# Kernel tuning notes

Measured on AMD Instinct MI355X. Metric: run time of the kernel, lower is better.

The kernel has to match this reference:

```python
import jax, jax.numpy as jnp
import numpy as np
import math

D_MODEL = 1024
NUM_HEADS = 16
B, L = 2, 2048
# scale_level=0, patch_time_span=1 -> effective_stride=1
PERIODS = (1.0, 30.0)
WEIGHTS = (0.8, 0.4)
SIGMAS = (0.5, 2.0)


def setup_inputs() -> dict:
    key = jax.random.key(0)
    ks = jax.random.split(key, 10)
    s = 1.0 / math.sqrt(D_MODEL)
    inp = {
        "x": jax.random.normal(ks[0], (B, L, D_MODEL), dtype=jnp.float32),
        "Wq": jax.random.normal(ks[1], (D_MODEL, D_MODEL), dtype=jnp.float32) * s,
        "bq": jax.random.normal(ks[2], (D_MODEL,), dtype=jnp.float32) * 0.01,
        "Wk": jax.random.normal(ks[3], (D_MODEL, D_MODEL), dtype=jnp.float32) * s,
        "bk": jax.random.normal(ks[4], (D_MODEL,), dtype=jnp.float32) * 0.01,
        "Wv": jax.random.normal(ks[5], (D_MODEL, D_MODEL), dtype=jnp.float32) * s,
        "bv": jax.random.normal(ks[6], (D_MODEL,), dtype=jnp.float32) * 0.01,
        "Wo": jax.random.normal(ks[7], (D_MODEL, D_MODEL), dtype=jnp.float32) * s,
        "bo": jax.random.normal(ks[8], (D_MODEL,), dtype=jnp.float32) * 0.01,
        "prior_lambda": jnp.asarray(2.0, dtype=jnp.float32),
    }
    return inp


def _gaussian_mask(length):
    idx = jnp.arange(length, dtype=jnp.float32)
    delta = jnp.abs(idx[:, None] - idx[None, :])  # [L, L]
    mask = jnp.zeros_like(delta)
    for p, w, sigma in zip(PERIODS, WEIGHTS, SIGMAS):
        if p < 0.2:
            continue
        mask = mask + w * jnp.exp(-((delta - p) ** 2) / (2.0 * sigma ** 2))
    return mask


def reference(x, Wq, bq, Wk, bk, Wv, bv, Wo, bo, prior_lambda):
    Bx, Lx, D = x.shape
    H = NUM_HEADS
    hd = D // H

    def split_heads(t):  # [B, L, D] -> [B, H, L, hd]
        return t.reshape(Bx, Lx, H, hd).transpose(0, 2, 1, 3)

    Q = split_heads(x @ Wq.T + bq)
    K = split_heads(x @ Wk.T + bk)
    V = split_heads(x @ Wv.T + bv)

    scores = jnp.einsum("bhqd,bhkd->bhqk", Q, K) / math.sqrt(hd)
    scores = scores + prior_lambda * _gaussian_mask(Lx)[None, None, :, :]
    attn = jax.nn.softmax(scores, axis=-1)
    out = jnp.einsum("bhqk,bhkd->bhqd", attn, V)
    out = out.transpose(0, 2, 1, 3).reshape(Bx, Lx, D)
    return out @ Wo.T + bo
```

## Files before the change

kernel.cpp:

```cpp
#include <hip/hip_runtime.h>

#define D_MODEL 1024
#define SEQ_L   2048
#define NHEADS  16
#define HDIM    64
#define NROWS   4096

#define QSCALE 0.18033688011112042f
#define LOG2E  1.4426950408889634f

#if __has_builtin(__builtin_amdgcn_exp2f)
#define EXP2F(x) __builtin_amdgcn_exp2f(x)
#else
#define EXP2F(x) __expf((x) * 0.6931471805599453f)
#endif

typedef __attribute__((ext_vector_type(8))) short short8;
typedef __attribute__((ext_vector_type(4))) short short4v;
typedef __attribute__((ext_vector_type(4))) float floatx4;
typedef __attribute__((ext_vector_type(4))) unsigned short ushort4v;
typedef unsigned short ushort;

static __device__ __forceinline__ ushort f2bf(float f) {
    unsigned int u = __float_as_uint(f);
    u += 0x7FFFu + ((u >> 16) & 1u);
    return (ushort)(u >> 16);
}

static __device__ __forceinline__ floatx4 mfma16(short8 a, short8 b, floatx4 c) {
    return __builtin_amdgcn_mfma_f32_16x16x32_bf16(a, b, c, 0, 0, 0);
}

static __device__ __forceinline__ void store8bf(ushort* dst, float4 a, float4 b) {
    uint4 pk;
    pk.x = (unsigned)f2bf(a.x) | ((unsigned)f2bf(a.y) << 16);
    pk.y = (unsigned)f2bf(a.z) | ((unsigned)f2bf(a.w) << 16);
    pk.z = (unsigned)f2bf(b.x) | ((unsigned)f2bf(b.y) << 16);
    pk.w = (unsigned)f2bf(b.z) | ((unsigned)f2bf(b.w) << 16);
    *(uint4*)dst = pk;
}

static __device__ __forceinline__ void gll16(const ushort* g, ushort* l) {
    __builtin_amdgcn_global_load_lds(
        (const __attribute__((address_space(1))) unsigned int*)(const unsigned int*)g,
        (__attribute__((address_space(3))) unsigned int*)(unsigned int*)l,
        16, 0, 0);
}

__global__ __launch_bounds__(256) void convert_bf16(
    const float* __restrict__ x,
    const float* __restrict__ wq, const float* __restrict__ wk,
    const float* __restrict__ wv, const float* __restrict__ wo,
    ushort* __restrict__ xb, ushort* __restrict__ wb3, ushort* __restrict__ wob)
{
    const int seg = blockIdx.y;
    const float* src;
    ushort* dst;
    int n;
    if      (seg == 0) { src = x;  dst = xb;                n = 4194304; }
    else if (seg == 1) { src = wq; dst = wb3;               n = 1048576; }
    else if (seg == 2) { src = wk; dst = wb3 + 1048576;     n = 1048576; }
    else if (seg == 3) { src = wv; dst = wb3 + 2097152;     n = 1048576; }
    else               { src = wo; dst = wob;               n = 1048576; }
    const int i = (blockIdx.x * 256 + threadIdx.x) * 8;
    if (i >= n) return;
    float4 a = *(const float4*)(src + i);
    float4 b = *(const float4*)(src + i + 4);
    store8bf(dst + i, a, b);
}

__global__ __launch_bounds__(256, 4) void gemm_qkv(
    const ushort* __restrict__ A, const ushort* __restrict__ B,
    const float* __restrict__ bq, const float* __restrict__ bk,
    const float* __restrict__ bv,
    ushort* __restrict__ Qo, ushort* __restrict__ Ko, ushort* __restrict__ Vo)
{
    __shared__ ushort As[64 * 64];
    __shared__ ushort Bs[128 * 64];

    const int tid  = threadIdx.x;
    const int w    = tid >> 6;
    const int lane = tid & 63;
    const int l15  = lane & 15;
    const int quad = lane >> 4;

    const int bm = blockIdx.y * 64;
    const int bn = blockIdx.x * 128;
    const int z  = blockIdx.x >> 3;

    const int ciA0 = tid,        ciA1 = tid + 256;
    const int rA0 = ciA0 >> 3,   rA1 = ciA1 >> 3;
    const int sA0i = ciA0 & 7,   sA1i = ciA1 & 7;
    const ushort* aP0 = A + (size_t)(bm + rA0) * 1024 + (sA0i ^ (rA0 & 7)) * 8;
    const ushort* aP1 = A + (size_t)(bm + rA1) * 1024 + (sA1i ^ (rA1 & 7)) * 8;
    ushort* lA0 = &As[rA0 * 64 + sA0i * 8];
    ushort* lA1 = &As[rA1 * 64 + sA1i * 8];

    const ushort* bP[4];
    ushort* lB[4];
#pragma unroll
    for (int p = 0; p < 4; p++) {
        const int ci = tid + p * 256;
        const int r = ci >> 3, s = ci & 7;
        bP[p] = B + (size_t)(bn + r) * 1024 + (s ^ (r & 7)) * 8;
        lB[p] = &Bs[r * 64 + s * 8];
    }

    const int x7 = l15 & 7;

    floatx4 acc[4][2];
#pragma unroll
    for (int i = 0; i < 4; i++)
#pragma unroll
        for (int j = 0; j < 2; j++) acc[i][j] = (floatx4){0.f, 0.f, 0.f, 0.f};

    for (int k0 = 0; k0 < 1024; k0 += 64) {
        __syncthreads();
        gll16(aP0 + k0, lA0);
        gll16(aP1 + k0, lA1);
#pragma unroll
        for (int p = 0; p < 4; p++) gll16(bP[p] + k0, lB[p]);
        __syncthreads();

#pragma unroll
        for (int kk = 0; kk < 2; kk++) {
            const int slot = ((kk * 4 + quad) ^ x7) * 8;
            short8 af[4], bf[2];
#pragma unroll
            for (int mi = 0; mi < 4; mi++)
                af[mi] = *(const short8*)&As[(mi * 16 + l15) * 64 + slot];
#pragma unroll
            for (int ni = 0; ni < 2; ni++)
                bf[ni] = *(const short8*)&Bs[(w * 32 + ni * 16 + l15) * 64 + slot];
            if (z == 2) {
#pragma unroll
                for (int mi = 0; mi < 4; mi++)
#pragma unroll
                    for (int ni = 0; ni < 2; ni++)
                        acc[mi][ni] = mfma16(af[mi], bf[ni], acc[mi][ni]);
            } else {
#pragma unroll
                for (int mi = 0; mi < 4; mi++)
#pragma unroll
                    for (int ni = 0; ni < 2; ni++)
                        acc[mi][ni] = mfma16(bf[ni], af[mi], acc[mi][ni]);
            }
        }
    }

    __syncthreads();
    ushort* St = Bs;
    const int cwbase = bn & 1023;
    const int bb = bm >> 11;

    if (z == 2) {
#pragma unroll
        for (int ni = 0; ni < 2; ni++) {
            const int hdp = w * 32 + ni * 16 + l15;
            const float bvl = bv[cwbase + hdp];
            const int xr = (hdp & 7) << 1;
#pragma unroll
            for (int mi = 0; mi < 4; mi++) {
                ushort4v pk;
#pragma unroll
                for (int r = 0; r < 4; r++) pk[r] = f2bf(acc[mi][ni][r] + bvl);
                const int gs = (mi * 4 + quad) ^ xr;
                *(ushort4v*)&St[hdp * 64 + gs * 4] = pk;
            }
        }
        __syncthreads();
        const int li0 = bm & 2047;
        const int c = lane & 7;
#pragma unroll
        for (int t = 0; t < 4; t++) {
            const int hdp = w * 32 + t * 8 + (lane >> 3);
            const int h  = (cwbase >> 6) + (hdp >> 6);
            const int hd = hdp & 63;
            const int gs = (2 * c) ^ ((hdp & 7) << 1);
            uint4 vdat = *(const uint4*)&St[hdp * 64 + gs * 4];
            *(uint4*)(Vo + ((size_t)(bb * NHEADS + h) * HDIM + hd) * SEQ_L + li0 + c * 8) = vdat;
        }
    } else {
        const float* bias = z ? bk : bq;
        const float scale = z ? 1.0f : QSCALE;
        ushort* outp = z ? Ko : Qo;
#pragma unroll
        for (int ni = 0; ni < 2; ni++) {
            const int colw = cwbase + w * 32 + ni * 16 + quad * 4;
            const float4 bb4 = *(const float4*)&bias[colw];
#pragma unroll
            for (int mi = 0; mi < 4; mi++) {
                const int row = mi * 16 + l15;
                ushort4v pk;
                pk[0] = f2bf((acc[mi][ni][0] + bb4.x) * scale);
                pk[1] = f2bf((acc[mi][ni][1] + bb4.y) * scale);
                pk[2] = f2bf((acc[mi][ni][2] + bb4.z) * scale);
                pk[3] = f2bf((acc[mi][ni][3] + bb4.w) * scale);
                const int gs = (w * 8 + ni * 4 + quad) ^ ((row & 7) << 2);
                *(ushort4v*)&St[row * 128 + gs * 4] = pk;
            }
        }
        __syncthreads();
        const int c = l15;
        const int h0 = cwbase >> 6;
        const int h  = h0 + (c >> 3);
        const int hd0 = (c & 7) * 8;
#pragma unroll
        for (int t = 0; t < 4; t++) {
            const int row = w * 16 + t * 4 + quad;
            const int li = (bm + row) & 2047;
            const int gs = (2 * c) ^ ((row & 7) << 2);
            uint4 vdat = *(const uint4*)&St[row * 128 + gs * 4];
            *(uint4*)(outp + ((size_t)(bb * NHEADS + h) * SEQ_L + li) * HDIM + hd0) = vdat;
        }
    }
}

__global__ __launch_bounds__(256, 4) void attn(
    const ushort* __restrict__ Q,
    const ushort* __restrict__ K,
    const ushort* __restrict__ Vt,
    const float* __restrict__ lam,
    ushort* __restrict__ O0, ushort* __restrict__ O1,
    float* __restrict__ Lw)
{
    __shared__ float mtab[128];
    __shared__ ushort Ks[2][64 * 64];
    __shared__ ushort Vts[2][64 * 64];

    const int tid  = threadIdx.x;
    const int wave = tid >> 6;
    const int lane = tid & 63;
    const int l15  = lane & 15;
    const int quad = lane >> 4;

    const int qb = blockIdx.x;
    const int h  = blockIdx.y;
    const int zz = blockIdx.z;
    const int bz = zz >> 1;
    const int sp = zz & 1;
    const int bh = bz * NHEADS + h;
    const int q0 = qb * 128;
    const int kb = sp * 1024;

    const float lambda = *lam;
    if (tid < 128) {
        float d  = (float)tid;
        float e1 = (d - 1.f) * (d - 1.f);
        float e2 = (d - 30.f) * (d - 30.f);
        mtab[tid] = LOG2E * lambda *
                    (0.8f * __expf(-2.0f * e1) + 0.4f * __expf(-0.125f * e2));
    }

    const ushort* qp =
        Q + ((size_t)bh * SEQ_L + q0 + wave * 16 + l15) * HDIM + quad * 8;
    short8 qf[2][2];
    qf[0][0] = *(const short8*)qp;
    qf[0][1] = *(const short8*)(qp + 32);
    qf[1][0] = *(const short8*)(qp + 64 * HDIM);
    qf[1][1] = *(const short8*)(qp + 64 * HDIM + 32);

    const ushort* kbase = K  + ((size_t)bh * SEQ_L) * HDIM;
    const ushort* vbase = Vt + ((size_t)bh * HDIM) * SEQ_L;

    const int cid0 = tid, cid1 = 256 + tid;
    const int row0 = cid0 >> 3, row1 = cid1 >> 3;
    const int cl0  = (cid0 & 7) ^ (row0 & 7);
    const int cl1  = (cid1 & 7) ^ (row1 & 7);
    const ushort* kg0 = kbase + (size_t)(kb + row0) * HDIM + cl0 * 8;
    const ushort* kg1 = kbase + (size_t)(kb + row1) * HDIM + cl1 * 8;
    const ushort* vg0 = vbase + (size_t)row0 * SEQ_L + kb + cl0 * 8;
    const ushort* vg1 = vbase + (size_t)row1 * SEQ_L + kb + cl1 * 8;

    floatx4 o[2][4];
#pragma unroll
    for (int g = 0; g < 2; g++)
#pragma unroll
        for (int i = 0; i < 4; i++) o[g][i] = (floatx4){0.f, 0.f, 0.f, 0.f};
    floatx4 ol[2];
    ol[0] = (floatx4){0.f, 0.f, 0.f, 0.f};
    ol[1] = (floatx4){0.f, 0.f, 0.f, 0.f};

    uint4 onesw;
    onesw.x = 0x3F803F80u; onesw.y = 0x3F803F80u;
    onesw.z = 0x3F803F80u; onesw.w = 0x3F803F80u;
    const short8 ones8 = __builtin_bit_cast(short8, onesw);

    gll16(kg0, &Ks[0][cid0 * 8]);
    gll16(kg1, &Ks[0][cid1 * 8]);
    gll16(vg0, &Vts[0][cid0 * 8]);
    gll16(vg1, &Vts[0][cid1 * 8]);

    const int xo = l15 & 7;

    for (int t = 0; t < 16; t++) {
        const int cur = t & 1;
        __syncthreads();
        if (t + 1 < 16) {
            const int nxt = cur ^ 1;
            const int koff = (t + 1) * 64;
            gll16(kg0 + (size_t)koff * HDIM, &Ks[nxt][cid0 * 8]);
            gll16(kg1 + (size_t)koff * HDIM, &Ks[nxt][cid1 * 8]);
            gll16(vg0 + koff, &Vts[nxt][cid0 * 8]);
            gll16(vg1 + koff, &Vts[nxt][cid1 * 8]);
        }

        floatx4 s[2][4];
#pragma unroll
        for (int g = 0; g < 2; g++)
#pragma unroll
            for (int i = 0; i < 4; i++) s[g][i] = (floatx4){0.f, 0.f, 0.f, 0.f};
#pragma unroll
        for (int kk = 0; kk < 2; kk++) {
#pragma unroll
            for (int nt = 0; nt < 4; nt++) {
                const int slot = (kk * 4 + quad) ^ xo;
                short8 kf = *(const short8*)&Ks[cur][(nt * 16 + l15) * 64 + slot * 8];
                s[0][nt] = mfma16(kf, qf[0][kk], s[0][nt]);
                s[1][nt] = mfma16(kf, qf[1][kk], s[1][nt]);
            }
        }

        const int j = sp * 16 + t;
#pragma unroll
        for (int g = 0; g < 2; g++) {
            const int tg = j - (qb * 2 + g);
            if (tg >= -1 && tg <= 1) {
                const int qg = q0 + g * 64 + wave * 16 + l15;
#pragma unroll
                for (int nt = 0; nt < 4; nt++) {
                    const int kgi = j * 64 + nt * 16 + quad * 4;
#pragma unroll
                    for (int r = 0; r < 4; r++) {
                        int dq = qg - (kgi + r);
                        int ad = dq < 0 ? -dq : dq;
                        s[g][nt][r] += mtab[ad];
                    }
                }
            }
        }

        short8 pb8[2][2];
#pragma unroll
        for (int g = 0; g < 2; g++) {
#pragma unroll
            for (int c = 0; c < 2; c++) {
                unsigned ur[8];
#pragma unroll
                for (int r = 0; r < 4; r++)
                    ur[r] = __float_as_uint(EXP2F(s[g][2 * c][r])) + 0x8000u;
#pragma unroll
                for (int r = 0; r < 4; r++)
                    ur[4 + r] = __float_as_uint(EXP2F(s[g][2 * c + 1][r])) + 0x8000u;
                uint4 pk;
                pk.x = __builtin_amdgcn_perm(ur[1], ur[0], 0x07060302u);
                pk.y = __builtin_amdgcn_perm(ur[3], ur[2], 0x07060302u);
                pk.z = __builtin_amdgcn_perm(ur[5], ur[4], 0x07060302u);
                pk.w = __builtin_amdgcn_perm(ur[7], ur[6], 0x07060302u);
                pb8[g][c] = __builtin_bit_cast(short8, pk);
            }
        }

#pragma unroll
        for (int c = 0; c < 2; c++) {
#pragma unroll
            for (int nt = 0; nt < 4; nt++) {
                const int glo = ((c << 2) + (quad >> 1)) ^ xo;
                const int ghi = glo ^ 2;
                const int rb  = (nt * 16 + l15) * 64 + (quad & 1) * 4;
                short4v vlo = *(const short4v*)&Vts[cur][rb + glo * 8];
                short4v vhi = *(const short4v*)&Vts[cur][rb + ghi * 8];
                short8 vf8 = __builtin_shufflevector(vlo, vhi, 0, 1, 2, 3, 4, 5, 6, 7);
                o[0][nt] = mfma16(vf8, pb8[0][c], o[0][nt]);
                o[1][nt] = mfma16(vf8, pb8[1][c], o[1][nt]);
            }
            ol[0] = mfma16(ones8, pb8[0][c], ol[0]);
            ol[1] = mfma16(ones8, pb8[1][c], ol[1]);
        }
    }

    ushort* Osp = sp ? O1 : O0;
#pragma unroll
    for (int g = 0; g < 2; g++) {
        const int qg = q0 + g * 64 + wave * 16 + l15;
        if (quad == 0)
            Lw[((size_t)(sp * 2 + bz) * NHEADS + h) * SEQ_L + qg] = ol[g][0];
        ushort* obase = Osp + ((size_t)bz * SEQ_L + qg) * D_MODEL + h * HDIM;
#pragma unroll
        for (int nt = 0; nt < 4; nt++) {
            ushort4v pk;
#pragma unroll
            for (int r = 0; r < 4; r++) pk[r] = f2bf(o[g][nt][r]);
            *(ushort4v*)(obase + nt * 16 + quad * 4) = pk;
        }
    }
}

__global__ __launch_bounds__(256) void merge_attn(
    const ushort* __restrict__ O0, const ushort* __restrict__ O1,
    const float* __restrict__ Lw, ushort* __restrict__ Aout)
{
    const int gid = blockIdx.x * 256 + threadIdx.x;
    const int i = gid * 8;
    const int row = i >> 10;
    const int h   = (i >> 6) & 15;
    const int bz  = row >> 11, q = row & 2047;
    const int li  = (bz * NHEADS + h) * SEQ_L + q;
    const float linv = 1.f / (Lw[li] + Lw[2 * NHEADS * SEQ_L + li]);

    uint4 a = *(const uint4*)(O0 + i);
    uint4 b = *(const uint4*)(O1 + i);
    unsigned aw[4] = {a.x, a.y, a.z, a.w};
    unsigned bw[4] = {b.x, b.y, b.z, b.w};
    uint4 res;
    unsigned rw[4];
#pragma unroll
    for (int k = 0; k < 4; k++) {
        float alo = __uint_as_float(aw[k] << 16);
        float ahi = __uint_as_float(aw[k] & 0xFFFF0000u);
        float blo = __uint_as_float(bw[k] << 16);
        float bhi = __uint_as_float(bw[k] & 0xFFFF0000u);
        float lo = (alo + blo) * linv;
        float hi = (ahi + bhi) * linv;
        rw[k] = (unsigned)f2bf(lo) | ((unsigned)f2bf(hi) << 16);
    }
    res.x = rw[0]; res.y = rw[1]; res.z = rw[2]; res.w = rw[3];
    *(uint4*)(Aout + i) = res;
}

__global__ __launch_bounds__(256, 4) void gemm_out(
    const ushort* __restrict__ A, const ushort* __restrict__ B,
    const float* __restrict__ bo, float* __restrict__ out)
{
    __shared__ ushort As[64 * 64];
    __shared__ ushort Bs[64 * 64];

    const int tid  = threadIdx.x;
    const int w    = tid >> 6;
    const int lane = tid & 63;
    const int l15  = lane & 15;
    const int quad = lane >> 4;

    const int bm = blockIdx.y * 64;
    const int bn = blockIdx.x * 64;

    const int ci0 = tid, ci1 = tid + 256;
    const int r0 = ci0 >> 3, r1 = ci1 >> 3;
    const int s0 = ci0 & 7,  s1 = ci1 & 7;
    const ushort* aP0 = A + (size_t)(bm + r0) * 1024 + (s0 ^ (r0 & 7)) * 8;
    const ushort* aP1 = A + (size_t)(bm + r1) * 1024 + (s1 ^ (r1 & 7)) * 8;
    const ushort* bP0 = B + (size_t)(bn + r0) * 1024 + (s0 ^ (r0 & 7)) * 8;
    const ushort* bP1 = B + (size_t)(bn + r1) * 1024 + (s1 ^ (r1 & 7)) * 8;
    ushort* lA0 = &As[r0 * 64 + s0 * 8];
    ushort* lA1 = &As[r1 * 64 + s1 * 8];
    ushort* lB0 = &Bs[r0 * 64 + s0 * 8];
    ushort* lB1 = &Bs[r1 * 64 + s1 * 8];

    const int x7 = l15 & 7;

    floatx4 acc[4];
#pragma unroll
    for (int i = 0; i < 4; i++) acc[i] = (floatx4){0.f, 0.f, 0.f, 0.f};

    for (int k0 = 0; k0 < 1024; k0 += 64) {
        __syncthreads();
        gll16(aP0 + k0, lA0);
        gll16(aP1 + k0, lA1);
        gll16(bP0 + k0, lB0);
        gll16(bP1 + k0, lB1);
        __syncthreads();

#pragma unroll
        for (int kk = 0; kk < 2; kk++) {
            const int slot = ((kk * 4 + quad) ^ x7) * 8;
            short8 bf = *(const short8*)&Bs[(w * 16 + l15) * 64 + slot];
#pragma unroll
            for (int mi = 0; mi < 4; mi++) {
                short8 af = *(const short8*)&As[(mi * 16 + l15) * 64 + slot];
                acc[mi] = mfma16(bf, af, acc[mi]);
            }
        }
    }

    const int col0 = bn + w * 16 + quad * 4;
    const float4 bb4 = *(const float4*)&bo[col0];
#pragma unroll
    for (int mi = 0; mi < 4; mi++) {
        const int row = bm + mi * 16 + l15;
        float4 st;
        st.x = acc[mi][0] + bb4.x;
        st.y = acc[mi][1] + bb4.y;
        st.z = acc[mi][2] + bb4.z;
        st.w = acc[mi][3] + bb4.w;
        *(float4*)(out + (size_t)row * 1024 + col0) = st;
    }
}

extern "C" void kernel_launch(void* const* d_in, const int* in_sizes, int n_in,
                              void* d_out, int out_size, void* d_ws, size_t ws_size,
                              hipStream_t stream)
{
    const float* x   = (const float*)d_in[0];
    const float* Wq  = (const float*)d_in[1];
    const float* bq  = (const float*)d_in[2];
    const float* Wk  = (const float*)d_in[3];
    const float* bk  = (const float*)d_in[4];
    const float* Wv  = (const float*)d_in[5];
    const float* bv  = (const float*)d_in[6];
    const float* Wo  = (const float*)d_in[7];
    const float* bo  = (const float*)d_in[8];
    const float* lam = (const float*)d_in[9];
    float* out = (float*)d_out;

    const size_t NELEM = (size_t)NROWS * D_MODEL;
    ushort* Qw  = (ushort*)d_ws;
    ushort* Kw  = Qw + NELEM;
    ushort* Vw  = Kw + NELEM;
    ushort* O0  = Vw + NELEM;
    ushort* O1  = O0 + NELEM;
    ushort* XA  = O1 + NELEM;
    ushort* Wb3 = XA + NELEM;
    ushort* Wob = Wb3 + 3 * 1024 * 1024;
    float*  Lw  = (float*)(Wob + 1024 * 1024);

    dim3 gc(2048, 5);
    convert_bf16<<<gc, 256, 0, stream>>>(x, Wq, Wk, Wv, Wo, XA, Wb3, Wob);

    dim3 g1(3072 / 128, NROWS / 64);
    gemm_qkv<<<g1, 256, 0, stream>>>(XA, Wb3, bq, bk, bv, Qw, Kw, Vw);

    dim3 g2(SEQ_L / 128, NHEADS, 4);
    attn<<<g2, 256, 0, stream>>>(Qw, Kw, Vw, lam, O0, O1, Lw);

    merge_attn<<<NELEM / (256 * 8), 256, 0, stream>>>(O0, O1, Lw, XA);

    dim3 g3(1024 / 64, NROWS / 64);
    gemm_out<<<g3, 256, 0, stream>>>(XA, Wob, bo, out);
}
```

Before: 197.2 us.

## Drop split-K attention and merge kernel; use 64-row query tiles over full keys

The attention kernel stops splitting the key range into two halves that write partial outputs and row sums for a separate merge pass. Each block now handles 64 query rows over all 2048 keys and normalises in-register before writing bf16 output straight into the GEMM input buffer. This removes the merge kernel launch and the partial-output traffic. In exchange, K/V tiles loaded into shared memory are reused by half as many query rows, and the serial loop per block is twice as long, though the grid block count stays the same.

```diff
diff --git a/kernel.cpp b/kernel.cpp
--- a/kernel.cpp
+++ b/kernel.cpp
@@ -221,8 +221,7 @@
     const ushort* __restrict__ K,
     const ushort* __restrict__ Vt,
     const float* __restrict__ lam,
-    ushort* __restrict__ O0, ushort* __restrict__ O1,
-    float* __restrict__ Lw)
+    ushort* __restrict__ Aout)
 {
     __shared__ float mtab[128];
     __shared__ ushort Ks[2][64 * 64];
@@ -236,12 +235,9 @@
 
     const int qb = blockIdx.x;
     const int h  = blockIdx.y;
-    const int zz = blockIdx.z;
-    const int bz = zz >> 1;
-    const int sp = zz & 1;
+    const int bz = blockIdx.z;
     const int bh = bz * NHEADS + h;
-    const int q0 = qb * 128;
-    const int kb = sp * 1024;
+    const int q0 = qb * 64;
 
     const float lambda = *lam;
     if (tid < 128) {
@@ -254,11 +250,9 @@
 
     const ushort* qp =
         Q + ((size_t)bh * SEQ_L + q0 + wave * 16 + l15) * HDIM + quad * 8;
-    short8 qf[2][2];
-    qf[0][0] = *(const short8*)qp;
-    qf[0][1] = *(const short8*)(qp + 32);
-    qf[1][0] = *(const short8*)(qp + 64 * HDIM);
-    qf[1][1] = *(const short8*)(qp + 64 * HDIM + 32);
+    short8 qf[2];
+    qf[0] = *(const short8*)qp;
+    qf[1] = *(const short8*)(qp + 32);
 
     const ushort* kbase = K  + ((size_t)bh * SEQ_L) * HDIM;
     const ushort* vbase = Vt + ((size_t)bh * HDIM) * SEQ_L;
@@ -267,19 +261,15 @@
     const int row0 = cid0 >> 3, row1 = cid1 >> 3;
     const int cl0  = (cid0 & 7) ^ (row0 & 7);
     const int cl1  = (cid1 & 7) ^ (row1 & 7);
-    const ushort* kg0 = kbase + (size_t)(kb + row0) * HDIM + cl0 * 8;
-    const ushort* kg1 = kbase + (size_t)(kb + row1) * HDIM + cl1 * 8;
-    const ushort* vg0 = vbase + (size_t)row0 * SEQ_L + kb + cl0 * 8;
-    const ushort* vg1 = vbase + (size_t)row1 * SEQ_L + kb + cl1 * 8;
-
-    floatx4 o[2][4];
-#pragma unroll
-    for (int g = 0; g < 2; g++)
-#pragma unroll
-        for (int i = 0; i < 4; i++) o[g][i] = (floatx4){0.f, 0.f, 0.f, 0.f};
-    floatx4 ol[2];
-    ol[0] = (floatx4){0.f, 0.f, 0.f, 0.f};
-    ol[1] = (floatx4){0.f, 0.f, 0.f, 0.f};
+    const ushort* kg0 = kbase + (size_t)row0 * HDIM + cl0 * 8;
+    const ushort* kg1 = kbase + (size_t)row1 * HDIM + cl1 * 8;
+    const ushort* vg0 = vbase + (size_t)row0 * SEQ_L + cl0 * 8;
+    const ushort* vg1 = vbase + (size_t)row1 * SEQ_L + cl1 * 8;
+
+    floatx4 o[4];
+#pragma unroll
+    for (int i = 0; i < 4; i++) o[i] = (floatx4){0.f, 0.f, 0.f, 0.f};
+    floatx4 ol = (floatx4){0.f, 0.f, 0.f, 0.f};
 
     uint4 onesw;
     onesw.x = 0x3F803F80u; onesw.y = 0x3F803F80u;
@@ -293,10 +283,10 @@
 
     const int xo = l15 & 7;
 
-    for (int t = 0; t < 16; t++) {
+    for (int t = 0; t < 32; t++) {
         const int cur = t & 1;
         __syncthreads();
-        if (t + 1 < 16) {
+        if (t + 1 < 32) {
             const int nxt = cur ^ 1;
             const int koff = (t + 1) * 64;
             gll16(kg0 + (size_t)koff * HDIM, &Ks[nxt][cid0 * 8]);
@@ -305,60 +295,50 @@
             gll16(vg1 + koff, &Vts[nxt][cid1 * 8]);
         }
 
-        floatx4 s[2][4];
-#pragma unroll
-        for (int g = 0; g < 2; g++)
-#pragma unroll
-            for (int i = 0; i < 4; i++) s[g][i] = (floatx4){0.f, 0.f, 0.f, 0.f};
+        floatx4 s[4];
+#pragma unroll
+        for (int i = 0; i < 4; i++) s[i] = (floatx4){0.f, 0.f, 0.f, 0.f};
 #pragma unroll
         for (int kk = 0; kk < 2; kk++) {
 #pragma unroll
             for (int nt = 0; nt < 4; nt++) {
                 const int slot = (kk * 4 + quad) ^ xo;
                 short8 kf = *(const short8*)&Ks[cur][(nt * 16 + l15) * 64 + slot * 8];
-                s[0][nt] = mfma16(kf, qf[0][kk], s[0][nt]);
-                s[1][nt] = mfma16(kf, qf[1][kk], s[1][nt]);
-            }
-        }
-
-        const int j = sp * 16 + t;
-#pragma unroll
-        for (int g = 0; g < 2; g++) {
-            const int tg = j - (qb * 2 + g);
-            if (tg >= -1 && tg <= 1) {
-                const int qg = q0 + g * 64 + wave * 16 + l15;
-#pragma unroll
-                for (int nt = 0; nt < 4; nt++) {
-                    const int kgi = j * 64 + nt * 16 + quad * 4;
-#pragma unroll
-                    for (int r = 0; r < 4; r++) {
-                        int dq = qg - (kgi + r);
-                        int ad = dq < 0 ? -dq : dq;
-                        s[g][nt][r] += mtab[ad];
-                    }
+                s[nt] = mfma16(kf, qf[kk], s[nt]);
+            }
+        }
+
+        const int tg = t - qb;
+        if (tg >= -1 && tg <= 1) {
+            const int qg = q0 + wave * 16 + l15;
+#pragma unroll
+            for (int nt = 0; nt < 4; nt++) {
+                const int kgi = t * 64 + nt * 16 + quad * 4;
+#pragma unroll
+                for (int r = 0; r < 4; r++) {
+                    int dq = qg - (kgi + r);
+                    int ad = dq < 0 ? -dq : dq;
+                    s[nt][r] += mtab[ad];
                 }
             }
         }
 
-        short8 pb8[2][2];
-#pragma unroll
-        for (int g = 0; g < 2; g++) {
-#pragma unroll
-            for (int c = 0; c < 2; c++) {
-                unsigned ur[8];
-#pragma unroll
-                for (int r = 0; r < 4; r++)
-                    ur[r] = __float_as_uint(EXP2F(s[g][2 * c][r])) + 0x8000u;
-#pragma unroll
-                for (int r = 0; r < 4; r++)
-                    ur[4 + r] = __float_as_uint(EXP2F(s[g][2 * c + 1][r])) + 0x8000u;
-                uint4 pk;
-                pk.x = __builtin_amdgcn_perm(ur[1], ur[0], 0x07060302u);
-                pk.y = __builtin_amdgcn_perm(ur[3], ur[2], 0x07060302u);
-                pk.z = __builtin_amdgcn_perm(ur[5], ur[4], 0x07060302u);
-                pk.w = __builtin_amdgcn_perm(ur[7], ur[6], 0x07060302u);
-                pb8[g][c] = __builtin_bit_cast(short8, pk);
-            }
+        short8 pb8[2];
+#pragma unroll
+        for (int c = 0; c < 2; c++) {
+            unsigned ur[8];
+#pragma unroll
+            for (int r = 0; r < 4; r++)
+                ur[r] = __float_as_uint(EXP2F(s[2 * c][r])) + 0x8000u;
+#pragma unroll
+            for (int r = 0; r < 4; r++)
+                ur[4 + r] = __float_as_uint(EXP2F(s[2 * c + 1][r])) + 0x8000u;
+            uint4 pk;
+            pk.x = __builtin_amdgcn_perm(ur[1], ur[0], 0x07060302u);
+            pk.y = __builtin_amdgcn_perm(ur[3], ur[2], 0x07060302u);
+            pk.z = __builtin_amdgcn_perm(ur[5], ur[4], 0x07060302u);
+            pk.w = __builtin_amdgcn_perm(ur[7], ur[6], 0x07060302u);
+            pb8[c] = __builtin_bit_cast(short8, pk);
         }
 
 #pragma unroll
@@ -371,61 +351,22 @@
                 short4v vlo = *(const short4v*)&Vts[cur][rb + glo * 8];
                 short4v vhi = *(const short4v*)&Vts[cur][rb + ghi * 8];
                 short8 vf8 = __builtin_shufflevector(vlo, vhi, 0, 1, 2, 3, 4, 5, 6, 7);
-                o[0][nt] = mfma16(vf8, pb8[0][c], o[0][nt]);
-                o[1][nt] = mfma16(vf8, pb8[1][c], o[1][nt]);
-            }
-            ol[0] = mfma16(ones8, pb8[0][c], ol[0]);
-            ol[1] = mfma16(ones8, pb8[1][c], ol[1]);
-        }
-    }
-
-    ushort* Osp = sp ? O1 : O0;
-#pragma unroll
-    for (int g = 0; g < 2; g++) {
-        const int qg = q0 + g * 64 + wave * 16 + l15;
-        if (quad == 0)
-            Lw[((size_t)(sp * 2 + bz) * NHEADS + h) * SEQ_L + qg] = ol[g][0];
-        ushort* obase = Osp + ((size_t)bz * SEQ_L + qg) * D_MODEL + h * HDIM;
-#pragma unroll
-        for (int nt = 0; nt < 4; nt++) {
-            ushort4v pk;
-#pragma unroll
-            for (int r = 0; r < 4; r++) pk[r] = f2bf(o[g][nt][r]);
-            *(ushort4v*)(obase + nt * 16 + quad * 4) = pk;
-        }
-    }
-}
-
-__global__ __launch_bounds__(256) void merge_attn(
-    const ushort* __restrict__ O0, const ushort* __restrict__ O1,
-    const float* __restrict__ Lw, ushort* __restrict__ Aout)
-{
-    const int gid = blockIdx.x * 256 + threadIdx.x;
-    const int i = gid * 8;
-    const int row = i >> 10;
-    const int h   = (i >> 6) & 15;
-    const int bz  = row >> 11, q = row & 2047;
-    const int li  = (bz * NHEADS + h) * SEQ_L + q;
-    const float linv = 1.f / (Lw[li] + Lw[2 * NHEADS * SEQ_L + li]);
-
-    uint4 a = *(const uint4*)(O0 + i);
-    uint4 b = *(const uint4*)(O1 + i);
-    unsigned aw[4] = {a.x, a.y, a.z, a.w};
-    unsigned bw[4] = {b.x, b.y, b.z, b.w};
-    uint4 res;
-    unsigned rw[4];
-#pragma unroll
-    for (int k = 0; k < 4; k++) {
-        float alo = __uint_as_float(aw[k] << 16);
-        float ahi = __uint_as_float(aw[k] & 0xFFFF0000u);
-        float blo = __uint_as_float(bw[k] << 16);
-        float bhi = __uint_as_float(bw[k] & 0xFFFF0000u);
-        float lo = (alo + blo) * linv;
-        float hi = (ahi + bhi) * linv;
-        rw[k] = (unsigned)f2bf(lo) | ((unsigned)f2bf(hi) << 16);
-    }
-    res.x = rw[0]; res.y = rw[1]; res.z = rw[2]; res.w = rw[3];
-    *(uint4*)(Aout + i) = res;
+                o[nt] = mfma16(vf8, pb8[c], o[nt]);
+            }
+            ol = mfma16(ones8, pb8[c], ol);
+        }
+    }
+
+    const float linv = 1.0f / ol[0];
+    const int qg = q0 + wave * 16 + l15;
+    ushort* obase = Aout + ((size_t)bz * SEQ_L + qg) * D_MODEL + h * HDIM;
+#pragma unroll
+    for (int nt = 0; nt < 4; nt++) {
+        ushort4v pk;
+#pragma unroll
+        for (int r = 0; r < 4; r++) pk[r] = f2bf(o[nt][r] * linv);
+        *(ushort4v*)(obase + nt * 16 + quad * 4) = pk;
+    }
 }
 
 __global__ __launch_bounds__(256, 4) void gemm_out(
@@ -516,12 +457,9 @@
     ushort* Qw  = (ushort*)d_ws;
     ushort* Kw  = Qw + NELEM;
     ushort* Vw  = Kw + NELEM;
-    ushort* O0  = Vw + NELEM;
-    ushort* O1  = O0 + NELEM;
-    ushort* XA  = O1 + NELEM;
+    ushort* XA  = Vw + NELEM;
     ushort* Wb3 = XA + NELEM;
     ushort* Wob = Wb3 + 3 * 1024 * 1024;
-    float*  Lw  = (float*)(Wob + 1024 * 1024);
 
     dim3 gc(2048, 5);
     convert_bf16<<<gc, 256, 0, stream>>>(x, Wq, Wk, Wv, Wo, XA, Wb3, Wob);
@@ -529,10 +467,8 @@
     dim3 g1(3072 / 128, NROWS / 64);
     gemm_qkv<<<g1, 256, 0, stream>>>(XA, Wb3, bq, bk, bv, Qw, Kw, Vw);
 
-    dim3 g2(SEQ_L / 128, NHEADS, 4);
-    attn<<<g2, 256, 0, stream>>>(Qw, Kw, Vw, lam, O0, O1, Lw);
-
-    merge_attn<<<NELEM / (256 * 8), 256, 0, stream>>>(O0, O1, Lw, XA);
+    dim3 g2(SEQ_L / 64, NHEADS, 2);
+    attn<<<g2, 256, 0, stream>>>(Qw, Kw, Vw, lam, XA);
 
     dim3 g3(1024 / 64, NROWS / 64);
     gemm_out<<<g3, 256, 0, stream>>>(XA, Wob, bo, out);
```

Result: slower. 204.2 us (+3.5%).
